# Kernel optimization log

Measured on AMD Instinct MI355X. Metric: run time of the kernel, lower is better.

Reference implementation:

```python
import jax, jax.numpy as jnp
import numpy as np

NUM_BINS = 256

def setup_inputs() -> dict:
    key = jax.random.key(0)
    k1, k2 = jax.random.split(key)
    B, C, H, W = 32, 3, 512, 512
    # images in [-1, 1], matching the torch module's denorm x*0.5+0.5
    imgs = jax.random.uniform(k1, (B, C, H, W), dtype=jnp.float32) * 2.0 - 1.0
    target_hist = jax.random.uniform(k2, (B, NUM_BINS), dtype=jnp.float32)
    return {"generated_img_batch": imgs, "target_hist_batch": target_hist}


def _batch_histograms(images, num_bins):
    # images: [B, C, H, W] in [-1, 1]
    B = images.shape[0]
    denorm = images * 0.5 + 0.5                       # [0, 1]
    idx = (denorm * (num_bins - 1)).astype(jnp.int32)  # [B, C, H, W]
    idx = idx.reshape(B, -1)                           # [B, C*H*W]
    rows = jnp.arange(B, dtype=jnp.int32)[:, None]
    hist = jnp.zeros((B, num_bins), dtype=jnp.float32)
    hist = hist.at[rows, idx].add(1.0)
    return hist


def reference(generated_img_batch, target_hist_batch):
    eps = 1e-8
    gen_hist = _batch_histograms(generated_img_batch, NUM_BINS)
    gen_p = gen_hist / (gen_hist.sum(axis=1, keepdims=True) + eps)
    tgt_p = target_hist_batch / (target_hist_batch.sum(axis=1, keepdims=True) + eps)
    gen_cdf = jnp.cumsum(gen_p, axis=1)
    tgt_cdf = jnp.cumsum(tgt_p, axis=1)
    return jnp.mean(jnp.abs(gen_cdf - tgt_cdf))
```

## Files before the change

### kernel.cpp

```cpp
#include <hip/hip_runtime.h>

#define NUM_BINS 256
#define BATCH 32
#define CHW (3 * 512 * 512)
#define N4 (CHW / 4)
#define BPB 64
#define ITERS (N4 / (BPB * 256))

#define GH_ELEMS (BATCH * BPB * NUM_BINS)

__global__ __launch_bounds__(256) void hist_kernel(
    const float* __restrict__ img, unsigned int* __restrict__ gh,
    unsigned int* __restrict__ counter) {
  __shared__ unsigned int lh[4][NUM_BINS];
  const int tid  = threadIdx.x;
  const int wave = tid >> 6;
  const int blk  = blockIdx.x;
  const int b    = blockIdx.y;

  if (blk == 0 && b == 0 && tid == 0) *counter = 0u;

  for (int i = tid; i < 4 * NUM_BINS; i += 256)
    ((unsigned int*)lh)[i] = 0u;
  __syncthreads();

  const float4* src = (const float4*)(img + (size_t)b * CHW);
  int i = blk * 256 + tid;
#pragma unroll 4
  for (int it = 0; it < ITERS; ++it, i += BPB * 256) {
    float4 v = src[i];
    int i0 = (int)((v.x * 0.5f + 0.5f) * 255.0f);
    int i1 = (int)((v.y * 0.5f + 0.5f) * 255.0f);
    int i2 = (int)((v.z * 0.5f + 0.5f) * 255.0f);
    int i3 = (int)((v.w * 0.5f + 0.5f) * 255.0f);
    i0 = min(max(i0, 0), NUM_BINS - 1);
    i1 = min(max(i1, 0), NUM_BINS - 1);
    i2 = min(max(i2, 0), NUM_BINS - 1);
    i3 = min(max(i3, 0), NUM_BINS - 1);
    atomicAdd(&lh[wave][i0], 1u);
    atomicAdd(&lh[wave][i1], 1u);
    atomicAdd(&lh[wave][i2], 1u);
    atomicAdd(&lh[wave][i3], 1u);
  }
  __syncthreads();

  unsigned int s = lh[0][tid] + lh[1][tid] + lh[2][tid] + lh[3][tid];
  gh[((size_t)b * BPB + blk) * NUM_BINS + tid] = s;
}

__global__ __launch_bounds__(256) void loss_kernel(
    const unsigned int* __restrict__ gh, const float* __restrict__ tgt,
    float* __restrict__ partial, unsigned int* __restrict__ counter,
    float* __restrict__ out) {
  __shared__ float wsum[4];
  __shared__ float wtot[4];
  __shared__ float wabs[4];
  __shared__ int last_flag;
  const int b = blockIdx.x, tid = threadIdx.x;
  const int lane = tid & 63, wave = tid >> 6;

  float t = tgt[b * NUM_BINS + tid];

  float g = 0.0f;
  const unsigned int* gb = gh + (size_t)b * BPB * NUM_BINS + tid;
#pragma unroll 8
  for (int k = 0; k < BPB; ++k) g += (float)gb[k * NUM_BINS];

  float st = t;
#pragma unroll
  for (int off = 32; off > 0; off >>= 1) st += __shfl_down(st, off);
  if (lane == 0) wsum[wave] = st;
  __syncthreads();
  float stT = wsum[0] + wsum[1] + wsum[2] + wsum[3];

  float v = g / (float)CHW - t / (stT + 1e-8f);

  float sv = v;
#pragma unroll
  for (int off = 1; off < 64; off <<= 1) {
    float n = __shfl_up(sv, off);
    if (lane >= off) sv += n;
  }
  if (lane == 63) wtot[wave] = sv;
  __syncthreads();
  float prefix = 0.0f;
  for (int w = 0; w < wave; ++w) prefix += wtot[w];
  sv += prefix;

  float a = fabsf(sv);
#pragma unroll
  for (int off = 32; off > 0; off >>= 1) a += __shfl_down(a, off);
  if (lane == 0) wabs[wave] = a;
  __syncthreads();

  if (tid == 0) {
    float tot = wabs[0] + wabs[1] + wabs[2] + wabs[3];
    atomicExch(&partial[b], tot);
    __threadfence();
    unsigned int old = atomicAdd(counter, 1u);
    last_flag = (old == BATCH - 1) ? 1 : 0;
  }
  __syncthreads();

  if (last_flag && wave == 0) {
    float pv = (lane < BATCH) ? atomicAdd(&partial[lane], 0.0f) : 0.0f;
#pragma unroll
    for (int off = 32; off > 0; off >>= 1) pv += __shfl_down(pv, off);
    if (lane == 0) out[0] = pv / (float)(BATCH * NUM_BINS);
  }
}

extern "C" void kernel_launch(void* const* d_in, const int* in_sizes, int n_in,
                              void* d_out, int out_size, void* d_ws, size_t ws_size,
                              hipStream_t stream) {
  const float* img = (const float*)d_in[0];
  const float* tgt = (const float*)d_in[1];
  float* out = (float*)d_out;

  unsigned int* gh = (unsigned int*)d_ws;
  float* partial = (float*)((char*)d_ws + GH_ELEMS * sizeof(unsigned int));
  unsigned int* counter = (unsigned int*)(partial + BATCH);

  dim3 hgrid(BPB, BATCH, 1);
  hist_kernel<<<hgrid, 256, 0, stream>>>(img, gh, counter);
  loss_kernel<<<BATCH, 256, 0, stream>>>(gh, tgt, partial, counter, out);
}
```

Baseline: 149.1 us.

## Use nontemporal image loads, drop index clamps, split loss reduction over 512 threads

The histogram kernel now reads the image through nontemporal vector loads and no longer clamps the bin indices, on the assumption that inputs stay within [-1,1]. The loss kernel runs 512 threads per batch, each half summing 32 of the 64 partial histograms before combining them in shared memory. This is meant to cut cache pollution and ALU work in the bandwidth-bound pass and halve the serial reduction length in the loss pass. Dropping the clamp risks out-of-bounds shared-memory atomics if any value falls outside the expected range.

```diff
diff --git a/kernel.cpp b/kernel.cpp
--- a/kernel.cpp
+++ b/kernel.cpp
@@ -8,6 +8,8 @@
 #define ITERS (N4 / (BPB * 256))
 
 #define GH_ELEMS (BATCH * BPB * NUM_BINS)
+
+typedef float f4 __attribute__((ext_vector_type(4)));
 
 __global__ __launch_bounds__(256) void hist_kernel(
     const float* __restrict__ img, unsigned int* __restrict__ gh,
@@ -24,19 +26,15 @@
     ((unsigned int*)lh)[i] = 0u;
   __syncthreads();
 
-  const float4* src = (const float4*)(img + (size_t)b * CHW);
+  const f4* src = (const f4*)(img + (size_t)b * CHW);
   int i = blk * 256 + tid;
 #pragma unroll 4
   for (int it = 0; it < ITERS; ++it, i += BPB * 256) {
-    float4 v = src[i];
+    f4 v = __builtin_nontemporal_load(&src[i]);
     int i0 = (int)((v.x * 0.5f + 0.5f) * 255.0f);
     int i1 = (int)((v.y * 0.5f + 0.5f) * 255.0f);
     int i2 = (int)((v.z * 0.5f + 0.5f) * 255.0f);
     int i3 = (int)((v.w * 0.5f + 0.5f) * 255.0f);
-    i0 = min(max(i0, 0), NUM_BINS - 1);
-    i1 = min(max(i1, 0), NUM_BINS - 1);
-    i2 = min(max(i2, 0), NUM_BINS - 1);
-    i3 = min(max(i3, 0), NUM_BINS - 1);
     atomicAdd(&lh[wave][i0], 1u);
     atomicAdd(&lh[wave][i1], 1u);
     atomicAdd(&lh[wave][i2], 1u);
@@ -44,27 +42,39 @@
   }
   __syncthreads();
 
-  unsigned int s = lh[0][tid] + lh[1][tid] + lh[2][tid] + lh[3][tid];
-  gh[((size_t)b * BPB + blk) * NUM_BINS + tid] = s;
+  if (tid < NUM_BINS) {
+    unsigned int s = lh[0][tid] + lh[1][tid] + lh[2][tid] + lh[3][tid];
+    gh[((size_t)b * BPB + blk) * NUM_BINS + tid] = s;
+  }
 }
 
-__global__ __launch_bounds__(256) void loss_kernel(
+__global__ __launch_bounds__(512) void loss_kernel(
     const unsigned int* __restrict__ gh, const float* __restrict__ tgt,
     float* __restrict__ partial, unsigned int* __restrict__ counter,
     float* __restrict__ out) {
-  __shared__ float wsum[4];
-  __shared__ float wtot[4];
-  __shared__ float wabs[4];
+  __shared__ float gsum[2][NUM_BINS];
+  __shared__ float wsum[8];
+  __shared__ float wtot[8];
+  __shared__ float wabs[8];
   __shared__ int last_flag;
   const int b = blockIdx.x, tid = threadIdx.x;
   const int lane = tid & 63, wave = tid >> 6;
-
-  float t = tgt[b * NUM_BINS + tid];
+  const int bin = tid & (NUM_BINS - 1);
+  const int half = tid >> 8;
 
   float g = 0.0f;
-  const unsigned int* gb = gh + (size_t)b * BPB * NUM_BINS + tid;
+  const unsigned int* gb =
+      gh + (size_t)b * BPB * NUM_BINS + (size_t)half * 32 * NUM_BINS + bin;
 #pragma unroll 8
-  for (int k = 0; k < BPB; ++k) g += (float)gb[k * NUM_BINS];
+  for (int k = 0; k < 32; ++k) g += (float)gb[k * NUM_BINS];
+  gsum[half][bin] = g;
+  __syncthreads();
+
+  float t = 0.0f, gt = 0.0f;
+  if (tid < NUM_BINS) {
+    t  = tgt[b * NUM_BINS + bin];
+    gt = gsum[0][bin] + gsum[1][bin];
+  }
 
   float st = t;
 #pragma unroll
@@ -73,7 +83,7 @@
   __syncthreads();
   float stT = wsum[0] + wsum[1] + wsum[2] + wsum[3];
 
-  float v = g / (float)CHW - t / (stT + 1e-8f);
+  float v = gt / (float)CHW - t / (stT + 1e-8f);
 
   float sv = v;
 #pragma unroll
@@ -84,10 +94,10 @@
   if (lane == 63) wtot[wave] = sv;
   __syncthreads();
   float prefix = 0.0f;
-  for (int w = 0; w < wave; ++w) prefix += wtot[w];
+  for (int w = 0; w < wave && w < 4; ++w) prefix += wtot[w];
   sv += prefix;
 
-  float a = fabsf(sv);
+  float a = (tid < NUM_BINS) ? fabsf(sv) : 0.0f;
 #pragma unroll
   for (int off = 32; off > 0; off >>= 1) a += __shfl_down(a, off);
   if (lane == 0) wabs[wave] = a;
@@ -123,5 +133,5 @@
 
   dim3 hgrid(BPB, BATCH, 1);
   hist_kernel<<<hgrid, 256, 0, stream>>>(img, gh, counter);
-  loss_kernel<<<BATCH, 256, 0, stream>>>(gh, tgt, partial, counter, out);
+  loss_kernel<<<BATCH, 512, 0, stream>>>(gh, tgt, partial, counter, out);
 }
```

New measurement: 142.5 us. 4.5% less time.
